# Kernel tuning notes

Hardware: AMD Instinct MI355X
Metric: run time of the kernel (lower is better)

The kernel has to match this reference:

```python
import jax, jax.numpy as jnp
import numpy as np

D_MODEL, D_K, D_V, N_HEADS = 1024, 64, 64, 16
B, S = 4, 4096
LN_EPS = 1e-5
NORM_EPS = 1e-12  # torch F.normalize default eps


def setup_inputs() -> dict:
    key = jax.random.key(0)
    ks = jax.random.split(key, 9)
    s = 0.02
    return {
        "x": jax.random.normal(ks[0], (B, S, D_MODEL), dtype=jnp.float32),
        # nn.Linear weights have shape [out, in]
        "W_Q": jax.random.normal(ks[1], (N_HEADS * D_K, D_MODEL), dtype=jnp.float32) * s,
        "W_K": jax.random.normal(ks[2], (N_HEADS * D_K, D_MODEL), dtype=jnp.float32) * s,
        "W_V": jax.random.normal(ks[3], (N_HEADS * D_V, D_MODEL), dtype=jnp.float32) * s,
        "W_g": jax.random.normal(ks[4], (N_HEADS * D_V, D_MODEL), dtype=jnp.float32) * s,
        "W_alpha": jax.random.normal(ks[5], (N_HEADS, D_MODEL), dtype=jnp.float32) * s,
        "W_O": jax.random.normal(ks[6], (D_MODEL, N_HEADS * D_V), dtype=jnp.float32) * s,
        "ln_gamma": jnp.ones((D_MODEL,), dtype=jnp.float32),
        "ln_beta": jnp.zeros((D_MODEL,), dtype=jnp.float32),
    }


def reference(x, W_Q, W_K, W_V, W_g, W_alpha, W_O, ln_gamma, ln_beta):
    # --- input projection chain (unfused variant) ---
    Q_raw = jnp.einsum('bsd,od->bso', x, W_Q)               # [B,S,H*Dk] (unused downstream)
    K_raw = jnp.einsum('bsd,od->bso', x, W_K)               # [B,S,H*Dk]
    V = jnp.einsum('bsd,od->bso', x, W_V)                   # [B,S,H*Dv]
    g_raw = jnp.einsum('bsd,od->bso', x, W_g)               # [B,S,H*Dv]
    alpha_raw = jnp.einsum('bsd,od->bso', x, W_alpha)       # [B,S,H]

    # F.normalize over the full last dim (n_heads*d_k), eps clamp on the norm
    K_norm = K_raw / jnp.maximum(jnp.linalg.norm(K_raw, axis=-1, keepdims=True), NORM_EPS)
    gate = jax.nn.silu(g_raw)
    alpha = jax.nn.sigmoid(alpha_raw)

    # scan is simulated as identity: scan_output = V
    scan_output = V

    # --- output epilogue: gate-multiply + output GEMM + residual + LayerNorm ---
    gated = scan_output * gate
    projected = jnp.einsum('bsv,dv->bsd', gated, W_O)
    pre = projected + x
    mean = jnp.mean(pre, axis=-1, keepdims=True)
    var = jnp.mean(jnp.square(pre - mean), axis=-1, keepdims=True)
    out = (pre - mean) * jax.lax.rsqrt(var + LN_EPS) * ln_gamma + ln_beta
    return out
```

## Files before the change

kernel.cpp:

```cpp
#include <hip/hip_runtime.h>

#define M_TOT 16384
#define DM    1024

typedef unsigned short ushort_t;
typedef __bf16 bf16x8 __attribute__((ext_vector_type(8)));
typedef float  f32x4  __attribute__((ext_vector_type(4)));

__device__ __forceinline__ ushort_t f32_to_bf16(float f) {
    union { float f; unsigned u; } v; v.f = f;
    unsigned u = v.u;
    return (ushort_t)((u + 0x7fffu + ((u >> 16) & 1u)) >> 16);
}
__device__ __forceinline__ float bf16_to_f32(ushort_t h) {
    union { unsigned u; float f; } v; v.u = ((unsigned)h) << 16;
    return v.f;
}

__device__ __forceinline__ void gload16(const ushort_t* g, ushort_t* l) {
    __builtin_amdgcn_global_load_lds(
        (const __attribute__((address_space(1))) unsigned int*)g,
        (__attribute__((address_space(3))) unsigned int*)l,
        16, 0, 0);
}

__global__ __launch_bounds__(256) void cvt_all(const float* __restrict__ x,
                                               const float* __restrict__ wv,
                                               const float* __restrict__ wg,
                                               const float* __restrict__ wo,
                                               ushort_t* __restrict__ xb,
                                               ushort_t* __restrict__ wcat,
                                               ushort_t* __restrict__ wob) {
    const long NX = (long)M_TOT * DM / 4, NW = (long)DM * DM / 4;
    long i = (long)blockIdx.x * 256 + threadIdx.x;
    const float* src; ushort_t* dst; long so, di;
    if (i < NX) {
        src = x; so = i; dst = xb; di = i;
    } else if (i < NX + NW) {
        long j = i - NX; src = wv; so = j;
        int row = (int)(j >> 8), c4 = (int)(j & 255);
        int orow = ((row >> 4) << 5) | (row & 15);
        dst = wcat; di = (long)orow * 256 + c4;
    } else if (i < NX + 2 * NW) {
        long j = i - NX - NW; src = wg; so = j;
        int row = (int)(j >> 8), c4 = (int)(j & 255);
        int orow = ((row >> 4) << 5) | 16 | (row & 15);
        dst = wcat; di = (long)orow * 256 + c4;
    } else {
        long j = i - NX - 2 * NW; src = wo; so = j; dst = wob; di = j;
    }
    const float4 v = ((const float4*)src)[so];
    ushort4 o;
    o.x = f32_to_bf16(v.x); o.y = f32_to_bf16(v.y);
    o.z = f32_to_bf16(v.z); o.w = f32_to_bf16(v.w);
    ((ushort4*)dst)[di] = o;
}

template<int EPI>
__global__ __launch_bounds__(512, 2) void gemm8p(
    const ushort_t* __restrict__ A,
    const ushort_t* __restrict__ B,
    const ushort_t* __restrict__ Xb,
    ushort_t* __restrict__ out,
    int nbs)
{
    extern __shared__ ushort_t lds[];

    const int flat = blockIdx.x;
    const int xcd  = flat & 7;
    const int ii   = flat >> 3;
    const int m0   = ((xcd << 3) + (ii >> nbs)) << 8;
    const int n0   = (ii & ((1 << nbs) - 1)) << 8;

    const int tid  = threadIdx.x;
    const int w    = tid >> 6;
    const int l    = tid & 63;
    const int wm   = w >> 2;
    const int wn   = w & 3;
    const int fr   = l & 15;
    const int quad = l >> 4;

    f32x4 acc[8][4];
    const f32x4 vzero = {0.f, 0.f, 0.f, 0.f};
#pragma unroll
    for (int i = 0; i < 8; ++i)
#pragma unroll
        for (int j = 0; j < 4; ++j) acc[i][j] = vzero;

    const int sA0 = (m0 + w * 16 + fr) * DM + (quad << 3);
    const int sA1 = sA0 + 128 * DM;
    const int sB0 = (n0 + w * 16 + fr) * DM + (quad << 3);
    const int sB1 = sB0 + 128 * DM;

    auto stageA = [&](int u) {
        const int d  = (u & 3) * 8192 + w * 512;
        const int ko = u * 32;
        gload16(A + sA0 + ko, lds + d);
        gload16(A + sA1 + ko, lds + d + 4096);
    };
    auto stageB = [&](int u) {
        const int d  = 32768 + (u & 3) * 8192 + w * 512;
        const int ko = u * 32;
        gload16(B + sB0 + ko, lds + d);
        gload16(B + sB1 + ko, lds + d + 4096);
    };

    const int rA = wm * 4096 + l * 8;
    const int rB = 32768 + wn * 2048 + l * 8;

    stageA(0); stageB(0);
    stageA(1); stageB(1);
    stageA(2); stageB(2);
    asm volatile("s_waitcnt vmcnt(8)" ::: "memory");
    __builtin_amdgcn_s_barrier();

    for (int u = 0; u < 32; ++u) {
        const int sb = (u & 3) * 8192;
        bf16x8 bf[4], af[4];

#pragma unroll
        for (int j = 0; j < 4; ++j) bf[j] = *(const bf16x8*)(lds + sb + rB + j * 512);
#pragma unroll
        for (int i = 0; i < 4; ++i) af[i] = *(const bf16x8*)(lds + sb + rA + i * 512);
        if (u < 29) stageA(u + 3);
        __builtin_amdgcn_sched_barrier(0);
        __builtin_amdgcn_s_barrier();
        __builtin_amdgcn_s_setprio(1);
#pragma unroll
        for (int j = 0; j < 4; ++j)
#pragma unroll
            for (int i = 0; i < 4; ++i)
                acc[i][j] = __builtin_amdgcn_mfma_f32_16x16x32_bf16(
                    af[i], bf[j], acc[i][j], 0, 0, 0);
        __builtin_amdgcn_s_setprio(0);
        __builtin_amdgcn_sched_barrier(0);
        __builtin_amdgcn_s_barrier();

#pragma unroll
        for (int i = 0; i < 4; ++i) af[i] = *(const bf16x8*)(lds + sb + rA + (4 + i) * 512);
        if (u < 29) stageB(u + 3);
        if (u < 29)       { asm volatile("s_waitcnt vmcnt(8)" ::: "memory"); }
        else if (u == 29) { asm volatile("s_waitcnt vmcnt(4)" ::: "memory"); }
        else if (u == 30) { asm volatile("s_waitcnt vmcnt(0)" ::: "memory"); }
        __builtin_amdgcn_sched_barrier(0);
        __builtin_amdgcn_s_barrier();
        __builtin_amdgcn_s_setprio(1);
#pragma unroll
        for (int j = 0; j < 4; ++j)
#pragma unroll
            for (int i = 0; i < 4; ++i)
                acc[4 + i][j] = __builtin_amdgcn_mfma_f32_16x16x32_bf16(
                    af[i], bf[j], acc[4 + i][j], 0, 0, 0);
        __builtin_amdgcn_s_setprio(0);
        __builtin_amdgcn_sched_barrier(0);
        __builtin_amdgcn_s_barrier();
    }

    const int rowb = m0 + wm * 128;
    const int colb = n0 + wn * 64;
    if (EPI == 0) {
#pragma unroll
        for (int i = 0; i < 8; ++i)
#pragma unroll
            for (int jp = 0; jp < 2; ++jp) {
                const int cb   = colb + jp * 32;
                const int vcol = ((cb >> 5) << 4) + fr;
#pragma unroll
                for (int r = 0; r < 4; ++r) {
                    const int row = rowb + i * 16 + quad * 4 + r;
                    float v = acc[i][2 * jp][r];
                    float g = acc[i][2 * jp + 1][r];
                    float gate = g / (1.0f + __expf(-g));
                    out[row * DM + vcol] = f32_to_bf16(v * gate);
                }
            }
    } else {
#pragma unroll
        for (int i = 0; i < 8; ++i)
#pragma unroll
            for (int j = 0; j < 4; ++j) {
                const int col = colb + j * 16 + fr;
#pragma unroll
                for (int r = 0; r < 4; ++r) {
                    const int row = rowb + i * 16 + quad * 4 + r;
                    float pre = acc[i][j][r] + bf16_to_f32(Xb[row * DM + col]);
                    out[row * DM + col] = f32_to_bf16(pre);
                }
            }
    }
}

__global__ __launch_bounds__(256) void ln_rows(const ushort_t* __restrict__ pre,
                                               const float* __restrict__ gamma,
                                               const float* __restrict__ beta,
                                               float* __restrict__ out)
{
    const int row = blockIdx.x;
    const int tid = threadIdx.x;
    const int wave = tid >> 6, lane = tid & 63;

    ushort4 u = ((const ushort4*)(pre + row * DM))[tid];
    float p0 = bf16_to_f32(u.x), p1 = bf16_to_f32(u.y);
    float p2 = bf16_to_f32(u.z), p3 = bf16_to_f32(u.w);

    float s  = p0 + p1 + p2 + p3;
    float ss = p0 * p0 + p1 * p1 + p2 * p2 + p3 * p3;
#pragma unroll
    for (int off = 32; off > 0; off >>= 1) {
        s  += __shfl_down(s, off);
        ss += __shfl_down(ss, off);
    }
    __shared__ float red[8];
    __shared__ float mb[2];
    if (lane == 0) { red[wave] = s; red[4 + wave] = ss; }
    __syncthreads();
    if (tid == 0) {
        float S  = red[0] + red[1] + red[2] + red[3];
        float SS = red[4] + red[5] + red[6] + red[7];
        float mean = S * (1.0f / 1024.0f);
        float var  = SS * (1.0f / 1024.0f) - mean * mean;
        mb[0] = mean;
        mb[1] = rsqrtf(var + 1e-5f);
    }
    __syncthreads();
    const float mean = mb[0], rs = mb[1];

    float4 gm = ((const float4*)gamma)[tid];
    float4 bt = ((const float4*)beta)[tid];
    float4 o;
    o.x = (p0 - mean) * rs * gm.x + bt.x;
    o.y = (p1 - mean) * rs * gm.y + bt.y;
    o.z = (p2 - mean) * rs * gm.z + bt.z;
    o.w = (p3 - mean) * rs * gm.w + bt.w;
    ((float4*)(out + row * DM))[tid] = o;
}

extern "C" void kernel_launch(void* const* d_in, const int* in_sizes, int n_in,
                              void* d_out, int out_size, void* d_ws, size_t ws_size,
                              hipStream_t stream) {
    const float* x     = (const float*)d_in[0];
    const float* WV    = (const float*)d_in[3];
    const float* WG    = (const float*)d_in[4];
    const float* WO    = (const float*)d_in[6];
    const float* gamma = (const float*)d_in[7];
    const float* beta  = (const float*)d_in[8];
    float* out = (float*)d_out;

    char* ws = (char*)d_ws;
    ushort_t* xb    = (ushort_t*)ws;
    ushort_t* gated = (ushort_t*)(ws + (size_t)M_TOT * DM * 2);
    ushort_t* wcat  = (ushort_t*)(ws + (size_t)M_TOT * DM * 4);
    ushort_t* wob   = (ushort_t*)(ws + (size_t)M_TOT * DM * 4 + (size_t)2 * DM * DM * 2);
    ushort_t* pre   = xb;

    static bool attr_set = false;
    if (!attr_set) {
        hipFuncSetAttribute((const void*)&gemm8p<0>,
                            hipFuncAttributeMaxDynamicSharedMemorySize, 131072);
        hipFuncSetAttribute((const void*)&gemm8p<1>,
                            hipFuncAttributeMaxDynamicSharedMemorySize, 131072);
        attr_set = true;
    }

    const int nCvt = (M_TOT * DM + 3 * DM * DM) / 4 / 256;
    cvt_all<<<nCvt, 256, 0, stream>>>(x, WV, WG, WO, xb, wcat, wob);

    gemm8p<0><<<512, 512, 131072, stream>>>(xb, wcat, nullptr, gated, 3);
    gemm8p<1><<<256, 512, 131072, stream>>>(gated, wob, xb, pre, 2);

    ln_rows<<<M_TOT, 256, 0, stream>>>(pre, gamma, beta, out);
}
```

Measured before the change: 274.5 us.

## Rewrite GEMMs with 32x32x16 MFMA, 256x128 tiles and triple-buffered LDS

Replaces the 512-thread 256x256-tile GEMM built on 16x16x32 MFMA with a 256-thread kernel using 256x128 tiles and 32x32x16 bf16 MFMA. LDS goes from four stages to a three-stage ring with a single barrier per k-step, and the V/gate weight interleave is reorganised to 32-row groups to match the new fragment layout. The aim is higher MFMA throughput per LDS read, fewer barriers, and less LDS per block so more blocks fit per CU. The cost is twice as many blocks, more A-tile reloads, and a different epilogue store pattern.

```diff
diff --git a/kernel.cpp b/kernel.cpp
--- a/kernel.cpp
+++ b/kernel.cpp
@@ -5,7 +5,7 @@
 
 typedef unsigned short ushort_t;
 typedef __bf16 bf16x8 __attribute__((ext_vector_type(8)));
-typedef float  f32x4  __attribute__((ext_vector_type(4)));
+typedef float  f32x16 __attribute__((ext_vector_type(16)));
 
 __device__ __forceinline__ ushort_t f32_to_bf16(float f) {
     union { float f; unsigned u; } v; v.f = f;
@@ -39,12 +39,12 @@
     } else if (i < NX + NW) {
         long j = i - NX; src = wv; so = j;
         int row = (int)(j >> 8), c4 = (int)(j & 255);
-        int orow = ((row >> 4) << 5) | (row & 15);
+        int orow = ((row >> 5) << 6) | (row & 31);
         dst = wcat; di = (long)orow * 256 + c4;
     } else if (i < NX + 2 * NW) {
         long j = i - NX - NW; src = wg; so = j;
         int row = (int)(j >> 8), c4 = (int)(j & 255);
-        int orow = ((row >> 4) << 5) | 16 | (row & 15);
+        int orow = ((row >> 5) << 6) | 32 | (row & 31);
         dst = wcat; di = (long)orow * 256 + c4;
     } else {
         long j = i - NX - 2 * NW; src = wo; so = j; dst = wob; di = j;
@@ -57,9 +57,9 @@
 }
 
 template<int EPI>
-__global__ __launch_bounds__(512, 2) void gemm8p(
+__global__ __launch_bounds__(256, 2) void gemm2b(
     const ushort_t* __restrict__ A,
-    const ushort_t* __restrict__ B,
+    const ushort_t* __restrict__ Bm,
     const ushort_t* __restrict__ Xb,
     ushort_t* __restrict__ out,
     int nbs)
@@ -70,121 +70,125 @@
     const int xcd  = flat & 7;
     const int ii   = flat >> 3;
     const int m0   = ((xcd << 3) + (ii >> nbs)) << 8;
-    const int n0   = (ii & ((1 << nbs) - 1)) << 8;
+    const int n0   = (ii & ((1 << nbs) - 1)) << 7;
 
     const int tid  = threadIdx.x;
     const int w    = tid >> 6;
     const int l    = tid & 63;
-    const int wm   = w >> 2;
-    const int wn   = w & 3;
-    const int fr   = l & 15;
-    const int quad = l >> 4;
-
-    f32x4 acc[8][4];
-    const f32x4 vzero = {0.f, 0.f, 0.f, 0.f};
-#pragma unroll
-    for (int i = 0; i < 8; ++i)
-#pragma unroll
-        for (int j = 0; j < 4; ++j) acc[i][j] = vzero;
-
-    const int sA0 = (m0 + w * 16 + fr) * DM + (quad << 3);
-    const int sA1 = sA0 + 128 * DM;
-    const int sB0 = (n0 + w * 16 + fr) * DM + (quad << 3);
-    const int sB1 = sB0 + 128 * DM;
-
-    auto stageA = [&](int u) {
-        const int d  = (u & 3) * 8192 + w * 512;
+    const int wm   = w >> 1;
+    const int wn   = w & 1;
+
+    f32x16 acc[4][2];
+#pragma unroll
+    for (int i = 0; i < 4; ++i)
+#pragma unroll
+        for (int j = 0; j < 2; ++j) acc[i][j] = (f32x16)(0.f);
+
+    long gsrcA[4], gsrcB[2];
+#pragma unroll
+    for (int t = 0; t < 4; ++t) {
+        const int q = w * 4 + t, f = q >> 1, kh = q & 1;
+        gsrcA[t] = (long)(m0 + (f << 5) + (l & 31)) * DM + (kh << 4) + ((l >> 5) << 3);
+    }
+#pragma unroll
+    for (int t = 0; t < 2; ++t) {
+        const int q = w * 2 + t, f = q >> 1, kh = q & 1;
+        gsrcB[t] = (long)(n0 + (f << 5) + (l & 31)) * DM + (kh << 4) + ((l >> 5) << 3);
+    }
+
+    auto stage = [&](int u, int s) {
         const int ko = u * 32;
-        gload16(A + sA0 + ko, lds + d);
-        gload16(A + sA1 + ko, lds + d + 4096);
+        const int aBase = s * 8192 + l * 8;
+        const int bBase = 24576 + s * 4096 + l * 8;
+#pragma unroll
+        for (int t = 0; t < 4; ++t)
+            gload16(A + gsrcA[t] + ko, lds + aBase + (w * 4 + t) * 512);
+#pragma unroll
+        for (int t = 0; t < 2; ++t)
+            gload16(Bm + gsrcB[t] + ko, lds + bBase + (w * 2 + t) * 512);
     };
-    auto stageB = [&](int u) {
-        const int d  = 32768 + (u & 3) * 8192 + w * 512;
-        const int ko = u * 32;
-        gload16(B + sB0 + ko, lds + d);
-        gload16(B + sB1 + ko, lds + d + 4096);
-    };
-
-    const int rA = wm * 4096 + l * 8;
-    const int rB = 32768 + wn * 2048 + l * 8;
-
-    stageA(0); stageB(0);
-    stageA(1); stageB(1);
-    stageA(2); stageB(2);
-    asm volatile("s_waitcnt vmcnt(8)" ::: "memory");
+
+    int rdA[4][2], rdB[2][2];
+#pragma unroll
+    for (int i = 0; i < 4; ++i)
+#pragma unroll
+        for (int kh = 0; kh < 2; ++kh)
+            rdA[i][kh] = ((wm * 4 + i) * 2 + kh) * 512 + l * 8;
+#pragma unroll
+    for (int j = 0; j < 2; ++j)
+#pragma unroll
+        for (int kh = 0; kh < 2; ++kh)
+            rdB[j][kh] = 24576 + ((wn * 2 + j) * 2 + kh) * 512 + l * 8;
+
+    stage(0, 0); stage(1, 1);
+    asm volatile("s_waitcnt vmcnt(6)" ::: "memory");
     __builtin_amdgcn_s_barrier();
 
+    int sC = 0, sS = 2;
     for (int u = 0; u < 32; ++u) {
-        const int sb = (u & 3) * 8192;
-        bf16x8 bf[4], af[4];
-
-#pragma unroll
-        for (int j = 0; j < 4; ++j) bf[j] = *(const bf16x8*)(lds + sb + rB + j * 512);
-#pragma unroll
-        for (int i = 0; i < 4; ++i) af[i] = *(const bf16x8*)(lds + sb + rA + i * 512);
-        if (u < 29) stageA(u + 3);
-        __builtin_amdgcn_sched_barrier(0);
-        __builtin_amdgcn_s_barrier();
-        __builtin_amdgcn_s_setprio(1);
-#pragma unroll
-        for (int j = 0; j < 4; ++j)
-#pragma unroll
-            for (int i = 0; i < 4; ++i)
-                acc[i][j] = __builtin_amdgcn_mfma_f32_16x16x32_bf16(
-                    af[i], bf[j], acc[i][j], 0, 0, 0);
-        __builtin_amdgcn_s_setprio(0);
-        __builtin_amdgcn_sched_barrier(0);
-        __builtin_amdgcn_s_barrier();
-
-#pragma unroll
-        for (int i = 0; i < 4; ++i) af[i] = *(const bf16x8*)(lds + sb + rA + (4 + i) * 512);
-        if (u < 29) stageB(u + 3);
-        if (u < 29)       { asm volatile("s_waitcnt vmcnt(8)" ::: "memory"); }
-        else if (u == 29) { asm volatile("s_waitcnt vmcnt(4)" ::: "memory"); }
+        const int ab = sC * 8192;
+        const int bb = sC * 4096;
+        bf16x8 af[4][2], bf[2][2];
+#pragma unroll
+        for (int j = 0; j < 2; ++j)
+#pragma unroll
+            for (int kh = 0; kh < 2; ++kh)
+                bf[j][kh] = *(const bf16x8*)(lds + bb + rdB[j][kh]);
+#pragma unroll
+        for (int i = 0; i < 4; ++i)
+#pragma unroll
+            for (int kh = 0; kh < 2; ++kh)
+                af[i][kh] = *(const bf16x8*)(lds + ab + rdA[i][kh]);
+
+        if (u < 30) stage(u + 2, sS);
+        asm volatile("s_waitcnt lgkmcnt(0)" ::: "memory");
+        if (u < 30)       { asm volatile("s_waitcnt vmcnt(6)" ::: "memory"); }
         else if (u == 30) { asm volatile("s_waitcnt vmcnt(0)" ::: "memory"); }
         __builtin_amdgcn_sched_barrier(0);
         __builtin_amdgcn_s_barrier();
+        __builtin_amdgcn_sched_barrier(0);
+
         __builtin_amdgcn_s_setprio(1);
 #pragma unroll
-        for (int j = 0; j < 4; ++j)
-#pragma unroll
-            for (int i = 0; i < 4; ++i)
-                acc[4 + i][j] = __builtin_amdgcn_mfma_f32_16x16x32_bf16(
-                    af[i], bf[j], acc[4 + i][j], 0, 0, 0);
+        for (int kh = 0; kh < 2; ++kh)
+#pragma unroll
+            for (int j = 0; j < 2; ++j)
+#pragma unroll
+                for (int i = 0; i < 4; ++i)
+                    acc[i][j] = __builtin_amdgcn_mfma_f32_32x32x16_bf16(
+                        af[i][kh], bf[j][kh], acc[i][j], 0, 0, 0);
         __builtin_amdgcn_s_setprio(0);
         __builtin_amdgcn_sched_barrier(0);
-        __builtin_amdgcn_s_barrier();
-    }
-
-    const int rowb = m0 + wm * 128;
-    const int colb = n0 + wn * 64;
+
+        if (++sC == 3) sC = 0;
+        if (++sS == 3) sS = 0;
+    }
+
+    const int rowb = m0 + wm * 128 + ((l >> 5) << 2);
     if (EPI == 0) {
-#pragma unroll
-        for (int i = 0; i < 8; ++i)
-#pragma unroll
-            for (int jp = 0; jp < 2; ++jp) {
-                const int cb   = colb + jp * 32;
-                const int vcol = ((cb >> 5) << 4) + fr;
-#pragma unroll
-                for (int r = 0; r < 4; ++r) {
-                    const int row = rowb + i * 16 + quad * 4 + r;
-                    float v = acc[i][2 * jp][r];
-                    float g = acc[i][2 * jp + 1][r];
-                    float gate = g / (1.0f + __expf(-g));
-                    out[row * DM + vcol] = f32_to_bf16(v * gate);
-                }
+        const int colv = ((n0 + wn * 64) >> 1) + (l & 31);
+#pragma unroll
+        for (int i = 0; i < 4; ++i)
+#pragma unroll
+            for (int r = 0; r < 16; ++r) {
+                const int row = rowb + i * 32 + (r & 3) + ((r >> 2) << 3);
+                float v = acc[i][0][r];
+                float g = acc[i][1][r];
+                float gate = g / (1.0f + __expf(-g));
+                out[(long)row * DM + colv] = f32_to_bf16(v * gate);
             }
     } else {
-#pragma unroll
-        for (int i = 0; i < 8; ++i)
-#pragma unroll
-            for (int j = 0; j < 4; ++j) {
-                const int col = colb + j * 16 + fr;
-#pragma unroll
-                for (int r = 0; r < 4; ++r) {
-                    const int row = rowb + i * 16 + quad * 4 + r;
-                    float pre = acc[i][j][r] + bf16_to_f32(Xb[row * DM + col]);
-                    out[row * DM + col] = f32_to_bf16(pre);
+        const int colb = n0 + wn * 64 + (l & 31);
+#pragma unroll
+        for (int i = 0; i < 4; ++i)
+#pragma unroll
+            for (int j = 0; j < 2; ++j) {
+                const int col = colb + j * 32;
+#pragma unroll
+                for (int r = 0; r < 16; ++r) {
+                    const int row = rowb + i * 32 + (r & 3) + ((r >> 2) << 3);
+                    float pre = acc[i][j][r] + bf16_to_f32(Xb[(long)row * DM + col]);
+                    out[(long)row * DM + col] = f32_to_bf16(pre);
                 }
             }
     }
@@ -255,18 +259,18 @@
 
     static bool attr_set = false;
     if (!attr_set) {
-        hipFuncSetAttribute((const void*)&gemm8p<0>,
-                            hipFuncAttributeMaxDynamicSharedMemorySize, 131072);
-        hipFuncSetAttribute((const void*)&gemm8p<1>,
-                            hipFuncAttributeMaxDynamicSharedMemorySize, 131072);
+        hipFuncSetAttribute((const void*)&gemm2b<0>,
+                            hipFuncAttributeMaxDynamicSharedMemorySize, 73728);
+        hipFuncSetAttribute((const void*)&gemm2b<1>,
+                            hipFuncAttributeMaxDynamicSharedMemorySize, 73728);
         attr_set = true;
     }
 
     const int nCvt = (M_TOT * DM + 3 * DM * DM) / 4 / 256;
     cvt_all<<<nCvt, 256, 0, stream>>>(x, WV, WG, WO, xb, wcat, wob);
 
-    gemm8p<0><<<512, 512, 131072, stream>>>(xb, wcat, nullptr, gated, 3);
-    gemm8p<1><<<256, 512, 131072, stream>>>(gated, wob, xb, pre, 2);
+    gemm2b<0><<<1024, 256, 73728, stream>>>(xb, wcat, nullptr, gated, 4);
+    gemm2b<1><<<512, 256, 73728, stream>>>(gated, wob, xb, pre, 3);
 
     ln_rows<<<M_TOT, 256, 0, stream>>>(pre, gamma, beta, out);
 }
```

New measurement: 305.8 us. +11.4%, slower.

## Interleave A/B LDS stages and move vmcnt wait after second MFMA block

Applied to the files above, without the earlier changes.

Changes the LDS layout so each pipeline stage stores A and B tiles together in one contiguous 16K-element slot instead of separate A and B regions. It moves the global-load wait from before the second MFMA half to after it, so loads have more time in flight, and removes several sched_barriers so the compiler has more freedom to schedule. It also switches address arithmetic to 64-bit. The removed scheduling fences and the later wait could let the compiler reorder LDS reads relative to the async global-to-LDS loads, which risks stalls or hazards.

```diff
diff --git a/kernel.cpp b/kernel.cpp
--- a/kernel.cpp
+++ b/kernel.cpp
@@ -57,9 +57,9 @@
 }
 
 template<int EPI>
-__global__ __launch_bounds__(512, 2) void gemm8p(
+__global__ __launch_bounds__(512, 2) void gemmS(
     const ushort_t* __restrict__ A,
-    const ushort_t* __restrict__ B,
+    const ushort_t* __restrict__ Bm,
     const ushort_t* __restrict__ Xb,
     ushort_t* __restrict__ out,
     int nbs)
@@ -87,26 +87,26 @@
 #pragma unroll
         for (int j = 0; j < 4; ++j) acc[i][j] = vzero;
 
-    const int sA0 = (m0 + w * 16 + fr) * DM + (quad << 3);
-    const int sA1 = sA0 + 128 * DM;
-    const int sB0 = (n0 + w * 16 + fr) * DM + (quad << 3);
-    const int sB1 = sB0 + 128 * DM;
+    const long sA0 = (long)(m0 + w * 16 + fr) * DM + (quad << 3);
+    const long sA1 = sA0 + 128 * (long)DM;
+    const long sB0 = (long)(n0 + w * 16 + fr) * DM + (quad << 3);
+    const long sB1 = sB0 + 128 * (long)DM;
 
     auto stageA = [&](int u) {
-        const int d  = (u & 3) * 8192 + w * 512;
+        const int d  = (u & 3) * 16384 + w * 512;
         const int ko = u * 32;
         gload16(A + sA0 + ko, lds + d);
         gload16(A + sA1 + ko, lds + d + 4096);
     };
     auto stageB = [&](int u) {
-        const int d  = 32768 + (u & 3) * 8192 + w * 512;
+        const int d  = (u & 3) * 16384 + 8192 + w * 512;
         const int ko = u * 32;
-        gload16(B + sB0 + ko, lds + d);
-        gload16(B + sB1 + ko, lds + d + 4096);
+        gload16(Bm + sB0 + ko, lds + d);
+        gload16(Bm + sB1 + ko, lds + d + 4096);
     };
 
     const int rA = wm * 4096 + l * 8;
-    const int rB = 32768 + wn * 2048 + l * 8;
+    const int rB = 8192 + wn * 2048 + l * 8;
 
     stageA(0); stageB(0);
     stageA(1); stageB(1);
@@ -115,15 +115,14 @@
     __builtin_amdgcn_s_barrier();
 
     for (int u = 0; u < 32; ++u) {
-        const int sb = (u & 3) * 8192;
-        bf16x8 bf[4], af[4];
+        const int sb = (u & 3) * 16384;
+        bf16x8 af[4], bf[4];
 
 #pragma unroll
         for (int j = 0; j < 4; ++j) bf[j] = *(const bf16x8*)(lds + sb + rB + j * 512);
 #pragma unroll
         for (int i = 0; i < 4; ++i) af[i] = *(const bf16x8*)(lds + sb + rA + i * 512);
         if (u < 29) stageA(u + 3);
-        __builtin_amdgcn_sched_barrier(0);
         __builtin_amdgcn_s_barrier();
         __builtin_amdgcn_s_setprio(1);
 #pragma unroll
@@ -133,16 +132,11 @@
                 acc[i][j] = __builtin_amdgcn_mfma_f32_16x16x32_bf16(
                     af[i], bf[j], acc[i][j], 0, 0, 0);
         __builtin_amdgcn_s_setprio(0);
-        __builtin_amdgcn_sched_barrier(0);
         __builtin_amdgcn_s_barrier();
 
 #pragma unroll
         for (int i = 0; i < 4; ++i) af[i] = *(const bf16x8*)(lds + sb + rA + (4 + i) * 512);
         if (u < 29) stageB(u + 3);
-        if (u < 29)       { asm volatile("s_waitcnt vmcnt(8)" ::: "memory"); }
-        else if (u == 29) { asm volatile("s_waitcnt vmcnt(4)" ::: "memory"); }
-        else if (u == 30) { asm volatile("s_waitcnt vmcnt(0)" ::: "memory"); }
-        __builtin_amdgcn_sched_barrier(0);
         __builtin_amdgcn_s_barrier();
         __builtin_amdgcn_s_setprio(1);
 #pragma unroll
@@ -152,6 +146,9 @@
                 acc[4 + i][j] = __builtin_amdgcn_mfma_f32_16x16x32_bf16(
                     af[i], bf[j], acc[4 + i][j], 0, 0, 0);
         __builtin_amdgcn_s_setprio(0);
+        if (u < 29)       { asm volatile("s_waitcnt vmcnt(8)" ::: "memory"); }
+        else if (u == 29) { asm volatile("s_waitcnt vmcnt(4)" ::: "memory"); }
+        else if (u == 30) { asm volatile("s_waitcnt vmcnt(0)" ::: "memory"); }
         __builtin_amdgcn_sched_barrier(0);
         __builtin_amdgcn_s_barrier();
     }
@@ -171,7 +168,7 @@
                     float v = acc[i][2 * jp][r];
                     float g = acc[i][2 * jp + 1][r];
                     float gate = g / (1.0f + __expf(-g));
-                    out[row * DM + vcol] = f32_to_bf16(v * gate);
+                    out[(long)row * DM + vcol] = f32_to_bf16(v * gate);
                 }
             }
     } else {
@@ -183,8 +180,8 @@
 #pragma unroll
                 for (int r = 0; r < 4; ++r) {
                     const int row = rowb + i * 16 + quad * 4 + r;
-                    float pre = acc[i][j][r] + bf16_to_f32(Xb[row * DM + col]);
-                    out[row * DM + col] = f32_to_bf16(pre);
+                    float pre = acc[i][j][r] + bf16_to_f32(Xb[(long)row * DM + col]);
+                    out[(long)row * DM + col] = f32_to_bf16(pre);
                 }
             }
     }
@@ -255,9 +252,9 @@
 
     static bool attr_set = false;
     if (!attr_set) {
-        hipFuncSetAttribute((const void*)&gemm8p<0>,
+        hipFuncSetAttribute((const void*)&gemmS<0>,
                             hipFuncAttributeMaxDynamicSharedMemorySize, 131072);
-        hipFuncSetAttribute((const void*)&gemm8p<1>,
+        hipFuncSetAttribute((const void*)&gemmS<1>,
                             hipFuncAttributeMaxDynamicSharedMemorySize, 131072);
         attr_set = true;
     }
@@ -265,8 +262,8 @@
     const int nCvt = (M_TOT * DM + 3 * DM * DM) / 4 / 256;
     cvt_all<<<nCvt, 256, 0, stream>>>(x, WV, WG, WO, xb, wcat, wob);
 
-    gemm8p<0><<<512, 512, 131072, stream>>>(xb, wcat, nullptr, gated, 3);
-    gemm8p<1><<<256, 512, 131072, stream>>>(gated, wob, xb, pre, 2);
+    gemmS<0><<<512, 512, 131072, stream>>>(xb, wcat, nullptr, gated, 3);
+    gemmS<1><<<256, 512, 131072, stream>>>(gated, wob, xb, pre, 2);
 
     ln_rows<<<M_TOT, 256, 0, stream>>>(pre, gamma, beta, out);
 }
```

Result: no change. 270.4 us (-1.5%).
